# Optimization experiments

Hardware: AMD Instinct MI355X
Metric: run time of the kernel (lower is better)

The kernel has to match this reference:

```python
import jax, jax.numpy as jnp
import numpy as np

N_PTS, N_NODES, N_CMP = 2048, 8192, 1024
CHUNK = 4  # cmp columns per scan step; bounds the [P, CHUNK, N] intermediate


def setup_inputs() -> dict:
    key = jax.random.key(0)
    k1, k2 = jax.random.split(key)
    x = jax.random.normal(k1, (N_PTS, N_NODES), dtype=jnp.float32)
    # learned edge states; EDG_NULL == 0, so mask = (states != 0)
    learned_edge_states = jax.random.randint(k2, (N_NODES, N_CMP), 0, 2, dtype=jnp.int32)
    return {"x": x, "learned_edge_states": learned_edge_states}


def _masked_colmax(x, mask):
    """x: [P, N] float; mask: [N, C] bool -> [P, C] max of x over masked nodes per column.

    Columns with no nonzero entries yield 0.0 (original leaves the zero-initialized output).
    Chunked over C to avoid materializing the full [P, N, C] tensor.
    """
    neg_inf = jnp.float32(-jnp.inf)
    P = x.shape[0]
    C = mask.shape[1]
    mask_chunks = mask.T.reshape(C // CHUNK, CHUNK, -1)  # [S, CHUNK, N]

    def step(carry, m):
        # m: [CHUNK, N]; masked max over node axis -> [P, CHUNK]
        vals = jnp.max(jnp.where(m[None, :, :], x[:, None, :], neg_inf), axis=2)
        return carry, vals

    _, out = jax.lax.scan(step, None, mask_chunks)  # [S, P, CHUNK]
    out = jnp.transpose(out, (1, 0, 2)).reshape(P, C)
    has_any = jnp.any(mask, axis=0)  # [C]
    return jnp.where(has_any[None, :], out, jnp.float32(0.0))


def reference(x, learned_edge_states):
    mask = learned_edge_states != 0
    return _masked_colmax(x, mask)
```

## Files before the change

kernel.cpp:

```cpp
#include <hip/hip_runtime.h>
#include <hip/hip_bf16.h>
#include <math.h>

#define N_PTS   2048
#define N_NODES 8192
#define N_CMP   1024
#define CAP     128
#define K_MIN   32
#define K_MAX   112


__device__ __forceinline__ unsigned int float_to_key(float f) {
    unsigned int b = __float_as_uint(f);
    return (b & 0x80000000u) ? ~b : (b | 0x80000000u);
}
__device__ __forceinline__ float key_to_float(unsigned int k) {
    unsigned int b = (k & 0x80000000u) ? (k ^ 0x80000000u) : ~k;
    return __uint_as_float(b);
}

__global__ __launch_bounds__(256) void fused_kernel(const float* __restrict__ x,
                                                    const int* __restrict__ states,
                                                    float* __restrict__ out) {
    int p    = blockIdx.x;
    int t    = threadIdx.x;
    int lane = t & 63;
    int w    = t >> 6;

    const float4* row4 = reinterpret_cast<const float4*>(x + (size_t)p * N_NODES);

    unsigned int key[32];
#pragma unroll
    for (int j = 0; j < 8; j++) {
        float4 v = row4[j * 256 + t];
        key[j * 4 + 0] = float_to_key(v.x);
        key[j * 4 + 1] = float_to_key(v.y);
        key[j * 4 + 2] = float_to_key(v.z);
        key[j * 4 + 3] = float_to_key(v.w);
    }

    __shared__ unsigned int s_cnt[2][4];
    __shared__ unsigned int s_red[4];
    __shared__ unsigned int s_key[CAP];
    __shared__ int          s_id[CAP];
    __shared__ float        s_sv[CAP];
    __shared__ int          s_sn[CAP];
    __shared__ int          s_num;

    unsigned int m = 0;
#pragma unroll
    for (int i = 0; i < 32; i++) m = max(m, key[i]);
#pragma unroll
    for (int d = 1; d < 64; d <<= 1)
        m = max(m, (unsigned int)__shfl_xor((int)m, d));
    if (lane == 0) s_red[w] = m;
    __syncthreads();
    unsigned int M = max(max(s_red[0], s_red[1]), max(s_red[2], s_red[3]));
    __syncthreads();

    unsigned int lo = 0, hi = M;
    for (int it = 0; it < 34; ++it) {
        if (hi - lo <= 1) break;
        unsigned int mid;
        if (it == 0) {
            mid = 0xC0200000u;
            if (mid >= hi) mid = hi - 1;
            if (mid <= lo) mid = lo + 1;
        } else {
            mid = lo + ((hi - lo) >> 1);
        }
        int myc = 0;
#pragma unroll
        for (int i = 0; i < 32; i++)
            myc += (int)__popcll(__ballot(key[i] >= mid));
        int par = it & 1;
        if (lane == 0) s_cnt[par][w] = (unsigned int)myc;
        __syncthreads();
        int c = (int)(s_cnt[par][0] + s_cnt[par][1] + s_cnt[par][2] + s_cnt[par][3]);
        if (c >= K_MIN) {
            lo = mid;
            if (c <= K_MAX) break;
        } else {
            hi = mid;
        }
    }
    unsigned int T = lo;

    if (t == 0) s_num = 0;
    __syncthreads();
#pragma unroll
    for (int i = 0; i < 32; i++) {
        if (key[i] >= T) {
            int pos = atomicAdd(&s_num, 1);
            if (pos < CAP) {
                s_key[pos] = key[i];
                s_id[pos]  = (i >> 2) * 1024 + (t << 2) + (i & 3);
            }
        }
    }
    __syncthreads();
    int L   = s_num;
    int len = (L > CAP) ? -1 : L;

    if (len > 0 && t < L) {
        unsigned int mk = s_key[t];
        int          mi = s_id[t];
        int r = 0;
        for (int j = 0; j < L; ++j) {
            unsigned int kj = s_key[j];
            r += (int)((kj > mk) | ((kj == mk) & (j < t)));
        }
        s_sv[r] = key_to_float(mk);
        s_sn[r] = mi;
    }
    __syncthreads();

    const int* srow_base = states;
#pragma unroll 1
    for (int i = 0; i < 4; ++i) {
        int cg = i * 4 + w;
        int c  = cg * 64 + lane;

        float res  = 0.0f;
        bool  done = false;

        if (len >= 0) {
#pragma unroll 1
            for (int k0 = 0; k0 < len; k0 += 8) {
                int kmax = len - k0;
                if (kmax > 8) kmax = 8;
                int sv[8];
#pragma unroll
                for (int j = 0; j < 8; j++) {
                    if (j < kmax) {
                        int n = __builtin_amdgcn_readfirstlane(s_sn[k0 + j]);
                        sv[j] = srow_base[(size_t)n * N_CMP + c];
                    }
                }
#pragma unroll
                for (int j = 0; j < 8; j++) {
                    if (j < kmax) {
                        bool hit = (sv[j] != 0);
                        if (!done && hit) { res = s_sv[k0 + j]; done = true; }
                    }
                }
                if (__all((int)done)) break;
            }
        }

        if (!done) {
            const float* row = x + (size_t)p * N_NODES;
            float mm = -INFINITY;
            for (int n = 0; n < N_NODES; n++) {
                if (srow_base[(size_t)n * N_CMP + c] != 0) mm = fmaxf(mm, row[n]);
            }
            res = (mm == -INFINITY) ? 0.0f : mm;
        }

        out[(size_t)p * N_CMP + c] = res;
    }
}

extern "C" void kernel_launch(void* const* d_in, const int* in_sizes, int n_in,
                              void* d_out, int out_size, void* d_ws, size_t ws_size,
                              hipStream_t stream) {
    const float* x      = (const float*)d_in[0];
    const int*   states = (const int*)d_in[1];
    float*       out    = (float*)d_out;

    fused_kernel<<<N_PTS, 256, 0, stream>>>(x, states, out);
}
```

Measured before the change: 130.5 us.

## Pack edge-state mask into bitset and use 1024-thread blocks per point

Adds a pre-pass kernel that packs the int32 edge-state matrix into a per-node bitset in workspace using wave ballots. The main kernel then probes candidate nodes by reading one 32-bit word per column instead of a full int32 per column, cutting gather traffic by up to 32x. It also widens blocks to 1024 threads so each thread owns one output column rather than looping over four. The cost is an extra launch and the pack pass over the 32 MB states array, plus a larger block whose barriers in the threshold search span 16 waves.

```diff
diff --git a/kernel.cpp b/kernel.cpp
--- a/kernel.cpp
+++ b/kernel.cpp
@@ -18,10 +18,36 @@
     unsigned int b = (k & 0x80000000u) ? (k ^ 0x80000000u) : ~k;
     return __uint_as_float(b);
 }
+__device__ __forceinline__ int col_word_off(int c) {
+    return (c >> 8) * 8 + (c & 3) * 2 + (((c >> 2) & 63) >> 5);
+}
+__device__ __forceinline__ int col_bit(int c) { return (c >> 2) & 31; }
 
-__global__ __launch_bounds__(256) void fused_kernel(const float* __restrict__ x,
-                                                    const int* __restrict__ states,
-                                                    float* __restrict__ out) {
+__global__ __launch_bounds__(256) void pack_kernel(const int4* __restrict__ states4,
+                                                   unsigned int* __restrict__ bitsT) {
+    int t    = threadIdx.x;
+    int lane = t & 63;
+    int W = blockIdx.x * 4 + (t >> 6);
+    int n = W >> 2;
+    int g = W & 3;
+    int4 v = states4[(size_t)n * 256 + g * 64 + lane];
+    unsigned long long b0 = __ballot(v.x != 0);
+    unsigned long long b1 = __ballot(v.y != 0);
+    unsigned long long b2 = __ballot(v.z != 0);
+    unsigned long long b3 = __ballot(v.w != 0);
+    if (lane == 0) {
+        uint4* dst = reinterpret_cast<uint4*>(bitsT + n * 32 + g * 8);
+        dst[0] = make_uint4((unsigned)b0, (unsigned)(b0 >> 32),
+                            (unsigned)b1, (unsigned)(b1 >> 32));
+        dst[1] = make_uint4((unsigned)b2, (unsigned)(b2 >> 32),
+                            (unsigned)b3, (unsigned)(b3 >> 32));
+    }
+}
+
+__global__ __launch_bounds__(1024) void fused_kernel(const float* __restrict__ x,
+                                                     const int* __restrict__ states,
+                                                     const unsigned int* __restrict__ bitsT,
+                                                     float* __restrict__ out) {
     int p    = blockIdx.x;
     int t    = threadIdx.x;
     int lane = t & 63;
@@ -29,18 +55,18 @@
 
     const float4* row4 = reinterpret_cast<const float4*>(x + (size_t)p * N_NODES);
 
-    unsigned int key[32];
+    unsigned int key[8];
 #pragma unroll
-    for (int j = 0; j < 8; j++) {
-        float4 v = row4[j * 256 + t];
+    for (int j = 0; j < 2; j++) {
+        float4 v = row4[j * 1024 + t];
         key[j * 4 + 0] = float_to_key(v.x);
         key[j * 4 + 1] = float_to_key(v.y);
         key[j * 4 + 2] = float_to_key(v.z);
         key[j * 4 + 3] = float_to_key(v.w);
     }
 
-    __shared__ unsigned int s_cnt[2][4];
-    __shared__ unsigned int s_red[4];
+    __shared__ unsigned int s_cnt[2][16];
+    __shared__ unsigned int s_red[16];
     __shared__ unsigned int s_key[CAP];
     __shared__ int          s_id[CAP];
     __shared__ float        s_sv[CAP];
@@ -49,13 +75,15 @@
 
     unsigned int m = 0;
 #pragma unroll
-    for (int i = 0; i < 32; i++) m = max(m, key[i]);
+    for (int i = 0; i < 8; i++) m = max(m, key[i]);
 #pragma unroll
     for (int d = 1; d < 64; d <<= 1)
         m = max(m, (unsigned int)__shfl_xor((int)m, d));
     if (lane == 0) s_red[w] = m;
     __syncthreads();
-    unsigned int M = max(max(s_red[0], s_red[1]), max(s_red[2], s_red[3]));
+    unsigned int M = 0;
+#pragma unroll
+    for (int i = 0; i < 16; i++) M = max(M, s_red[i]);
     __syncthreads();
 
     unsigned int lo = 0, hi = M;
@@ -71,12 +99,14 @@
         }
         int myc = 0;
 #pragma unroll
-        for (int i = 0; i < 32; i++)
+        for (int i = 0; i < 8; i++)
             myc += (int)__popcll(__ballot(key[i] >= mid));
         int par = it & 1;
         if (lane == 0) s_cnt[par][w] = (unsigned int)myc;
         __syncthreads();
-        int c = (int)(s_cnt[par][0] + s_cnt[par][1] + s_cnt[par][2] + s_cnt[par][3]);
+        int c = 0;
+#pragma unroll
+        for (int i = 0; i < 16; i++) c += (int)s_cnt[par][i];
         if (c >= K_MIN) {
             lo = mid;
             if (c <= K_MAX) break;
@@ -89,12 +119,12 @@
     if (t == 0) s_num = 0;
     __syncthreads();
 #pragma unroll
-    for (int i = 0; i < 32; i++) {
+    for (int i = 0; i < 8; i++) {
         if (key[i] >= T) {
             int pos = atomicAdd(&s_num, 1);
             if (pos < CAP) {
                 s_key[pos] = key[i];
-                s_id[pos]  = (i >> 2) * 1024 + (t << 2) + (i & 3);
+                s_id[pos]  = (i >> 2) * 4096 + (t << 2) + (i & 3);
             }
         }
     }
@@ -115,58 +145,54 @@
     }
     __syncthreads();
 
-    const int* srow_base = states;
+    int c    = w * 64 + lane;
+    int woff = col_word_off(c);
+    int bit  = col_bit(c);
+
+    float res  = 0.0f;
+    bool  done = false;
+
+    if (len >= 0) {
 #pragma unroll 1
-    for (int i = 0; i < 4; ++i) {
-        int cg = i * 4 + w;
-        int c  = cg * 64 + lane;
+        for (int k0 = 0; k0 < len; k0 += 16) {
+            int kmax = len - k0;
+            if (kmax > 16) kmax = 16;
+            unsigned int wb[16];
+#pragma unroll
+            for (int j = 0; j < 16; j++)
+                if (j < kmax) wb[j] = bitsT[s_sn[k0 + j] * 32 + woff];
+#pragma unroll
+            for (int j = 0; j < 16; j++) {
+                if (j < kmax) {
+                    bool hit = (wb[j] >> bit) & 1u;
+                    if (!done && hit) { res = s_sv[k0 + j]; done = true; }
+                }
+            }
+            if (__all((int)done)) break;
+        }
+    }
 
-        float res  = 0.0f;
-        bool  done = false;
+    if (!done) {
+        const float* row = x + (size_t)p * N_NODES;
+        float mm = -INFINITY;
+        for (int n = 0; n < N_NODES; n++) {
+            if (states[(size_t)n * N_CMP + c] != 0) mm = fmaxf(mm, row[n]);
+        }
+        res = (mm == -INFINITY) ? 0.0f : mm;
+    }
 
-        if (len >= 0) {
-#pragma unroll 1
-            for (int k0 = 0; k0 < len; k0 += 8) {
-                int kmax = len - k0;
-                if (kmax > 8) kmax = 8;
-                int sv[8];
-#pragma unroll
-                for (int j = 0; j < 8; j++) {
-                    if (j < kmax) {
-                        int n = __builtin_amdgcn_readfirstlane(s_sn[k0 + j]);
-                        sv[j] = srow_base[(size_t)n * N_CMP + c];
-                    }
-                }
-#pragma unroll
-                for (int j = 0; j < 8; j++) {
-                    if (j < kmax) {
-                        bool hit = (sv[j] != 0);
-                        if (!done && hit) { res = s_sv[k0 + j]; done = true; }
-                    }
-                }
-                if (__all((int)done)) break;
-            }
-        }
-
-        if (!done) {
-            const float* row = x + (size_t)p * N_NODES;
-            float mm = -INFINITY;
-            for (int n = 0; n < N_NODES; n++) {
-                if (srow_base[(size_t)n * N_CMP + c] != 0) mm = fmaxf(mm, row[n]);
-            }
-            res = (mm == -INFINITY) ? 0.0f : mm;
-        }
-
-        out[(size_t)p * N_CMP + c] = res;
-    }
+    out[(size_t)p * N_CMP + c] = res;
 }
 
 extern "C" void kernel_launch(void* const* d_in, const int* in_sizes, int n_in,
                               void* d_out, int out_size, void* d_ws, size_t ws_size,
                               hipStream_t stream) {
-    const float* x      = (const float*)d_in[0];
-    const int*   states = (const int*)d_in[1];
-    float*       out    = (float*)d_out;
+    const float* x       = (const float*)d_in[0];
+    const int*   states  = (const int*)d_in[1];
+    const int4*  states4 = (const int4*)d_in[1];
+    float*       out     = (float*)d_out;
+    unsigned int* bitsT  = (unsigned int*)d_ws;
 
-    fused_kernel<<<N_PTS, 256, 0, stream>>>(x, states, out);
+    pack_kernel<<<N_NODES * 4 / 4, 256, 0, stream>>>(states4, bitsT);
+    fused_kernel<<<N_PTS, 1024, 0, stream>>>(x, states, bitsT, out);
 }
```

After: 141.5 us. 8.4% more time.

## Pack edge-state mask into bitmask and replace sorted early-exit with masked max

Applied to the files above, without the earlier changes.

A new pre-pass kernel packs the int32 edge-state matrix into a per-node bitmask of 32 words, which is 32x smaller than reading int32 states. The main kernel drops the in-shared-memory rank sort of candidate values and the early-exit scan. Each column instead takes a masked max over all candidates, reading bits from the packed mask. This removes the sort, one barrier and most state-matrix traffic, at the cost of an extra launch and always scanning every candidate instead of stopping at the first hit.

```diff
diff --git a/kernel.cpp b/kernel.cpp
--- a/kernel.cpp
+++ b/kernel.cpp
@@ -19,8 +19,24 @@
     return __uint_as_float(b);
 }
 
+__global__ __launch_bounds__(256) void pack_kernel(const int* __restrict__ states,
+                                                   unsigned int* __restrict__ bitsT) {
+    int t    = threadIdx.x;
+    int lane = t & 63;
+    int W    = blockIdx.x * 4 + (t >> 6);
+    int n    = W >> 4;
+    int cg   = W & 15;
+    int s    = states[(size_t)n * N_CMP + cg * 64 + lane];
+    unsigned long long m = __ballot(s != 0);
+    if (lane == 0) {
+        bitsT[n * 32 + cg * 2]     = (unsigned int)(m & 0xffffffffull);
+        bitsT[n * 32 + cg * 2 + 1] = (unsigned int)(m >> 32);
+    }
+}
+
 __global__ __launch_bounds__(256) void fused_kernel(const float* __restrict__ x,
                                                     const int* __restrict__ states,
+                                                    const unsigned int* __restrict__ bitsT,
                                                     float* __restrict__ out) {
     int p    = blockIdx.x;
     int t    = threadIdx.x;
@@ -41,10 +57,8 @@
 
     __shared__ unsigned int s_cnt[2][4];
     __shared__ unsigned int s_red[4];
-    __shared__ unsigned int s_key[CAP];
-    __shared__ int          s_id[CAP];
-    __shared__ float        s_sv[CAP];
-    __shared__ int          s_sn[CAP];
+    __shared__ float        s_v[CAP];
+    __shared__ int          s_n[CAP];
     __shared__ int          s_num;
 
     unsigned int m = 0;
@@ -56,7 +70,6 @@
     if (lane == 0) s_red[w] = m;
     __syncthreads();
     unsigned int M = max(max(s_red[0], s_red[1]), max(s_red[2], s_red[3]));
-    __syncthreads();
 
     unsigned int lo = 0, hi = M;
     for (int it = 0; it < 34; ++it) {
@@ -93,8 +106,8 @@
         if (key[i] >= T) {
             int pos = atomicAdd(&s_num, 1);
             if (pos < CAP) {
-                s_key[pos] = key[i];
-                s_id[pos]  = (i >> 2) * 1024 + (t << 2) + (i & 3);
+                s_v[pos] = key_to_float(key[i]);
+                s_n[pos] = (i >> 2) * 1024 + (t << 2) + (i & 3);
             }
         }
     }
@@ -102,62 +115,36 @@
     int L   = s_num;
     int len = (L > CAP) ? -1 : L;
 
-    if (len > 0 && t < L) {
-        unsigned int mk = s_key[t];
-        int          mi = s_id[t];
-        int r = 0;
-        for (int j = 0; j < L; ++j) {
-            unsigned int kj = s_key[j];
-            r += (int)((kj > mk) | ((kj == mk) & (j < t)));
-        }
-        s_sv[r] = key_to_float(mk);
-        s_sn[r] = mi;
-    }
-    __syncthreads();
-
-    const int* srow_base = states;
 #pragma unroll 1
     for (int i = 0; i < 4; ++i) {
         int cg = i * 4 + w;
         int c  = cg * 64 + lane;
 
-        float res  = 0.0f;
-        bool  done = false;
-
+        float res = -INFINITY;
         if (len >= 0) {
-#pragma unroll 1
-            for (int k0 = 0; k0 < len; k0 += 8) {
-                int kmax = len - k0;
-                if (kmax > 8) kmax = 8;
-                int sv[8];
-#pragma unroll
-                for (int j = 0; j < 8; j++) {
-                    if (j < kmax) {
-                        int n = __builtin_amdgcn_readfirstlane(s_sn[k0 + j]);
-                        sv[j] = srow_base[(size_t)n * N_CMP + c];
-                    }
-                }
-#pragma unroll
-                for (int j = 0; j < 8; j++) {
-                    if (j < kmax) {
-                        bool hit = (sv[j] != 0);
-                        if (!done && hit) { res = s_sv[k0 + j]; done = true; }
-                    }
-                }
-                if (__all((int)done)) break;
+#pragma unroll 4
+            for (int k = 0; k < len; ++k) {
+                int n = __builtin_amdgcn_readfirstlane(s_n[k]);
+                unsigned int blo = bitsT[n * 32 + cg * 2];
+                unsigned int bhi = bitsT[n * 32 + cg * 2 + 1];
+                unsigned int ws  = (lane < 32) ? blo : bhi;
+                if ((ws >> (lane & 31)) & 1u) res = fmaxf(res, s_v[k]);
             }
         }
 
-        if (!done) {
+        float r;
+        if (res == -INFINITY) {
             const float* row = x + (size_t)p * N_NODES;
             float mm = -INFINITY;
             for (int n = 0; n < N_NODES; n++) {
-                if (srow_base[(size_t)n * N_CMP + c] != 0) mm = fmaxf(mm, row[n]);
+                if (states[(size_t)n * N_CMP + c] != 0) mm = fmaxf(mm, row[n]);
             }
-            res = (mm == -INFINITY) ? 0.0f : mm;
+            r = (mm == -INFINITY) ? 0.0f : mm;
+        } else {
+            r = res;
         }
 
-        out[(size_t)p * N_CMP + c] = res;
+        out[(size_t)p * N_CMP + c] = r;
     }
 }
 
@@ -167,6 +154,8 @@
     const float* x      = (const float*)d_in[0];
     const int*   states = (const int*)d_in[1];
     float*       out    = (float*)d_out;
+    unsigned int* bitsT = (unsigned int*)d_ws;
 
-    fused_kernel<<<N_PTS, 256, 0, stream>>>(x, states, out);
+    pack_kernel<<<(N_NODES * (N_CMP / 64)) / 4, 256, 0, stream>>>(states, bitsT);
+    fused_kernel<<<N_PTS, 256, 0, stream>>>(x, states, bitsT, out);
 }
```

Measured after the change: 227.3 us. +74.2%, slower.
